# Kernel tuning notes

Measured on AMD Instinct MI355X. Metric: run time of the kernel, lower is better.

The kernel has to match this reference:

```python
import jax, jax.numpy as jnp
import numpy as np

N_EMBED = 1024
N_HEAD = 16
HEAD_DIM = N_EMBED // N_HEAD


def setup_inputs() -> dict:
    key = jax.random.key(0)
    ks = jax.random.split(key, 5)
    s = 1.0 / np.sqrt(N_EMBED)
    return {
        "x": jax.random.normal(ks[0], (4, 2048, N_EMBED), dtype=jnp.float32),
        "W_kqv": jax.random.normal(ks[1], (3 * N_EMBED, N_EMBED), dtype=jnp.float32) * s,
        "b_kqv": jax.random.normal(ks[2], (3 * N_EMBED,), dtype=jnp.float32) * s,
        "W_proj": jax.random.normal(ks[3], (N_EMBED, N_EMBED), dtype=jnp.float32) * s,
        "b_proj": jax.random.normal(ks[4], (N_EMBED,), dtype=jnp.float32) * s,
    }


def reference(x, W_kqv, b_kqv, W_proj, b_proj):
    B, S, E = x.shape
    H, D = N_HEAD, E // N_HEAD
    kqv = x @ W_kqv.T + b_kqv  # [B,S,3E]
    # torch code splits as k, q, v (in that order)
    k, q, v = jnp.split(kqv, 3, axis=-1)
    to_heads = lambda t: t.reshape(B, S, H, D).transpose(0, 2, 1, 3)  # [B,H,S,D]
    k, q, v = to_heads(k), to_heads(q), to_heads(v)
    scale = 1.0 / np.sqrt(D).astype(np.float32)
    attn = jnp.einsum("bhqd,bhkd->bhqk", q, k) * scale
    causal = jnp.tril(jnp.ones((S, S), dtype=bool))
    attn = jnp.where(causal, attn, -jnp.inf)
    attn = jax.nn.softmax(attn, axis=-1)
    # dropout: eval mode (identity) for deterministic reference
    y = jnp.einsum("bhqk,bhkd->bhqd", attn, v)
    y = y.transpose(0, 2, 1, 3).reshape(B, S, E)
    return y @ W_proj.T + b_proj
```

## Files before the change

kernel.cpp:

```cpp
#include <hip/hip_runtime.h>
#include <cstddef>
#include <cstdint>

#define EMB 1024
#define NH 16
#define HD 64
#define BATCH 4
#define SEQ 2048
#define MROWS (BATCH * SEQ)

typedef __attribute__((ext_vector_type(8))) short bf16x8;
typedef __attribute__((ext_vector_type(4))) float f32x4;

__device__ __forceinline__ unsigned short f2bf(float f) {
    union { float f; unsigned int i; } c; c.f = f;
    return (unsigned short)((c.i + 0x7FFFu + ((c.i >> 16) & 1u)) >> 16);
}
__device__ __forceinline__ unsigned short f2bfr(float f) {
    union { float f; unsigned int i; } c; c.f = f;
    return (unsigned short)((c.i + 0x8000u) >> 16);
}

#define GLOAD_LDS16(gp, lp) __builtin_amdgcn_global_load_lds(                  \
    (const __attribute__((address_space(1))) void*)(gp),                       \
    (__attribute__((address_space(3))) void*)(lp), 16, 0, 0)

__global__ __launch_bounds__(256) void cvt_all(
    const float* __restrict__ x, const float* __restrict__ wk,
    const float* __restrict__ wp, unsigned short* __restrict__ xh,
    unsigned short* __restrict__ wkh, unsigned short* __restrict__ wph) {
    const int A = (BATCH * SEQ * EMB) / 4;
    const int B2 = (3 * EMB * EMB) / 4;
    const int C = (EMB * EMB) / 4;
    const int tot = A + B2 + C;
    const int stride = gridDim.x * blockDim.x;
    for (int i = blockIdx.x * blockDim.x + threadIdx.x; i < tot; i += stride) {
        const float* s; unsigned short* d; int j;
        if (i < A)            { s = x;  d = xh;  j = i; }
        else if (i < A + B2)  { s = wk; d = wkh; j = i - A; }
        else                  { s = wp; d = wph; j = i - A - B2; }
        const float4 v = ((const float4*)s)[j];
        ushort4 h;
        h.x = f2bf(v.x); h.y = f2bf(v.y); h.z = f2bf(v.z); h.w = f2bf(v.w);
        ((ushort4*)d)[j] = h;
    }
}

__device__ __forceinline__ void stage_tile(const unsigned short* __restrict__ src,
                                           int row0, int kt,
                                           unsigned short* lds, int wave, int lane) {
#pragma unroll
    for (int i = 0; i < 2; ++i) {
        const int c = wave * 2 + i;
        const int r = c * 16 + (lane >> 2);
        const int kq = (lane & 3) * 8;
        GLOAD_LDS16(src + (size_t)(row0 + r) * 1024 + kt + kq, lds + c * 512);
    }
}

__global__ __launch_bounds__(256) void gemm_qkv_mfma(
    const unsigned short* __restrict__ xh, const unsigned short* __restrict__ wh,
    const float* __restrict__ bias,
    unsigned short* __restrict__ Ko, unsigned short* __restrict__ Qo,
    unsigned short* __restrict__ Vo) {
    __shared__ unsigned short Ah[128 * 32];
    __shared__ unsigned short Bh[128 * 32];

    const int t = threadIdx.x, lane = t & 63, w = t >> 6;
    const int wr = w >> 1, wc = w & 1;
    const int g8 = (lane >> 4) * 8, g4 = (lane >> 4) * 4, l15 = lane & 15;

    const int nwg = 64 * 24;
    const int lin = blockIdx.x + gridDim.x * blockIdx.y;
    const int swz = (lin & 7) * (nwg >> 3) + (lin >> 3);
    const int m0 = (swz & 63) * 128, n0 = (swz >> 6) * 128;

    f32x4 acc[4][4] = {};

    for (int kt = 0; kt < 1024; kt += 32) {
        stage_tile(xh, m0, kt, Ah, w, lane);
        stage_tile(wh, n0, kt, Bh, w, lane);
        __syncthreads();

        bf16x8 a[4], bb[4];
#pragma unroll
        for (int m = 0; m < 4; ++m)
            a[m] = *(const bf16x8*)&Ah[(wr * 64 + m * 16 + l15) * 32 + g8];
#pragma unroll
        for (int n = 0; n < 4; ++n)
            bb[n] = *(const bf16x8*)&Bh[(wc * 64 + n * 16 + l15) * 32 + g8];
#pragma unroll
        for (int m = 0; m < 4; ++m)
#pragma unroll
            for (int n = 0; n < 4; ++n)
                acc[m][n] = __builtin_amdgcn_mfma_f32_16x16x32_bf16(a[m], bb[n], acc[m][n], 0, 0, 0);
        __syncthreads();
    }

#pragma unroll
    for (int n = 0; n < 4; ++n) {
        const int col = n0 + wc * 64 + n * 16 + l15;
        const float bv = bias[col];
        const int which = col >> 10;
        unsigned short* outp = (which == 0) ? Ko : (which == 1 ? Qo : Vo);
        const int cm = col & 1023, h = cm >> 6, d = cm & 63;
#pragma unroll
        for (int m = 0; m < 4; ++m)
#pragma unroll
            for (int jj = 0; jj < 4; ++jj) {
                const int row = m0 + wr * 64 + m * 16 + g4 + jj;
                const int b = row >> 11, s = row & 2047;
                outp[(((size_t)(b * NH + h) * SEQ + s) << 6) + d] =
                    f2bf(acc[m][n][jj] + bv);
            }
    }
}

__global__ __launch_bounds__(256) void gemm_proj_mfma(
    const unsigned short* __restrict__ Yb, const unsigned short* __restrict__ wh,
    const float* __restrict__ bias, float* __restrict__ Out) {
    __shared__ unsigned short Ah[128 * 32];
    __shared__ unsigned short Bh[128 * 32];

    const int t = threadIdx.x, lane = t & 63, w = t >> 6;
    const int wr = w >> 1, wc = w & 1;
    const int g8 = (lane >> 4) * 8, g4 = (lane >> 4) * 4, l15 = lane & 15;

    const int nwg = 64 * 8;
    const int lin = blockIdx.x + gridDim.x * blockIdx.y;
    const int swz = (lin & 7) * (nwg >> 3) + (lin >> 3);
    const int m0 = (swz & 63) * 128, n0 = (swz >> 6) * 128;

    f32x4 acc[4][4] = {};

    for (int kt = 0; kt < 1024; kt += 32) {
        stage_tile(Yb, m0, kt, Ah, w, lane);
        stage_tile(wh, n0, kt, Bh, w, lane);
        __syncthreads();

        bf16x8 a[4], bb[4];
#pragma unroll
        for (int m = 0; m < 4; ++m)
            a[m] = *(const bf16x8*)&Ah[(wr * 64 + m * 16 + l15) * 32 + g8];
#pragma unroll
        for (int n = 0; n < 4; ++n)
            bb[n] = *(const bf16x8*)&Bh[(wc * 64 + n * 16 + l15) * 32 + g8];
#pragma unroll
        for (int m = 0; m < 4; ++m)
#pragma unroll
            for (int n = 0; n < 4; ++n)
                acc[m][n] = __builtin_amdgcn_mfma_f32_16x16x32_bf16(a[m], bb[n], acc[m][n], 0, 0, 0);
        __syncthreads();
    }

#pragma unroll
    for (int n = 0; n < 4; ++n) {
        const int col = n0 + wc * 64 + n * 16 + l15;
        const float bv = bias[col];
#pragma unroll
        for (int m = 0; m < 4; ++m)
#pragma unroll
            for (int jj = 0; jj < 4; ++jj) {
                const int row = m0 + wr * 64 + m * 16 + g4 + jj;
                Out[(size_t)row * EMB + col] = acc[m][n][jj] + bv;
            }
    }
}

__global__ __launch_bounds__(256, 2) void attn_mfma(
    const unsigned short* __restrict__ Kt, const unsigned short* __restrict__ Qt,
    const unsigned short* __restrict__ Vg, unsigned short* __restrict__ Y) {
    __shared__ unsigned short Ks[128][72];
    __shared__ unsigned short Vs[64][136];
    __shared__ unsigned short Ps[128][136];

    const int lin = blockIdx.x;
    const int swz = (lin & 7) * 64 + (lin >> 3);
    const int pair = swz & 7, bh = swz >> 3;
    const int b = bh >> 4, h = bh & 15;
    const unsigned short* Qp = Qt + ((size_t)bh * SEQ << 6);
    const unsigned short* Kp = Kt + ((size_t)bh * SEQ << 6);
    const unsigned short* Vp = Vg + ((size_t)bh * SEQ << 6);

    const int t = threadIdx.x, lane = t & 63, w = t >> 6;
    const int hi = lane >> 4, l15 = lane & 15, g8 = hi * 8;
    const float SCL = 0.125f * 1.44269504f;

    union U8 { uint4 q; unsigned short u[8]; };
    U8 kreg[4], vreg[4];
    auto loadKV = [&](int tile) {
#pragma unroll
        for (int i = 0; i < 4; ++i) {
            const int c = t + (i << 8);
            const int r = c >> 3, col = (c & 7) * 8;
            kreg[i].q = *(const uint4*)(Kp + ((size_t)tile << 13) + r * 64 + col);
            vreg[i].q = *(const uint4*)(Vp + ((size_t)tile << 13) + r * 64 + col);
        }
    };

#pragma unroll 1
    for (int ph = 0; ph < 2; ++ph) {
        const int qt = ph ? (15 - pair) : pair;
        const int ntiles = qt + 1;
        const int q0 = qt * 128 + w * 32;

        bf16x8 qf[2][2];
#pragma unroll
        for (int rb = 0; rb < 2; ++rb)
#pragma unroll
            for (int kc = 0; kc < 2; ++kc)
                qf[rb][kc] = *(const bf16x8*)(
                    Qp + ((size_t)(q0 + rb * 16 + l15) << 6) + kc * 32 + g8);

        float lsum[2] = {0.f, 0.f};
        f32x4 o_acc[2][4] = {};

        loadKV(0);
#pragma unroll 1
        for (int tile = 0; tile < ntiles; ++tile) {
            __syncthreads();
#pragma unroll
            for (int i = 0; i < 4; ++i) {
                const int c = t + (i << 8);
                const int r = c >> 3, col = (c & 7) * 8;
                *(uint4*)&Ks[r][col] = kreg[i].q;
#pragma unroll
                for (int j = 0; j < 8; ++j) {
                    const int d = col + j;
                    Vs[d][r ^ (d & 56)] = vreg[i].u[j];
                }
            }
            if (tile + 1 < ntiles) loadKV(tile + 1);
            __syncthreads();

            const bool diag = (tile == ntiles - 1);
            const int kvb = tile << 7;

            __builtin_amdgcn_s_setprio(1);
#pragma unroll
            for (int n = 0; n < 8; ++n) {
                const bf16x8 kf0 = *(const bf16x8*)&Ks[n * 16 + l15][g8];
                const bf16x8 kf1 = *(const bf16x8*)&Ks[n * 16 + l15][32 + g8];
                f32x4 t0 = {}, t1 = {};
                t0 = __builtin_amdgcn_mfma_f32_16x16x32_bf16(kf0, qf[0][0], t0, 0, 0, 0);
                t0 = __builtin_amdgcn_mfma_f32_16x16x32_bf16(kf1, qf[0][1], t0, 0, 0, 0);
                t1 = __builtin_amdgcn_mfma_f32_16x16x32_bf16(kf0, qf[1][0], t1, 0, 0, 0);
                t1 = __builtin_amdgcn_mfma_f32_16x16x32_bf16(kf1, qf[1][1], t1, 0, 0, 0);
#pragma unroll
                for (int rb = 0; rb < 2; ++rb) {
                    const f32x4 tt = rb ? t1 : t0;
                    const int qrow = q0 + rb * 16 + l15;
                    unsigned int pk[2];
#pragma unroll
                    for (int jp = 0; jp < 2; ++jp) {
                        float v0 = fmaf(tt[2 * jp], SCL, -8.0f);
                        float v1 = fmaf(tt[2 * jp + 1], SCL, -8.0f);
                        if (diag) {
                            const int kv = kvb + n * 16 + 4 * hi + 2 * jp;
                            if (kv > qrow)     v0 = -1e30f;
                            if (kv + 1 > qrow) v1 = -1e30f;
                        }
                        const float p0 = exp2f(v0), p1 = exp2f(v1);
                        lsum[rb] += p0 + p1;
                        pk[jp] = (unsigned int)f2bfr(p0) |
                                 ((unsigned int)f2bfr(p1) << 16);
                    }
                    *(uint2*)&Ps[w * 32 + rb * 16 + l15][n * 16 + 4 * hi] =
                        make_uint2(pk[0], pk[1]);
                }
            }

#pragma unroll
            for (int kc = 0; kc < 4; ++kc) {
                bf16x8 vf[4];
#pragma unroll
                for (int nd = 0; nd < 4; ++nd) {
                    const int d = nd * 16 + l15;
                    vf[nd] = *(const bf16x8*)&Vs[d][(kc * 32 + g8) ^ (d & 56)];
                }
                const bf16x8 pf0 = *(const bf16x8*)&Ps[w * 32 + l15][kc * 32 + g8];
                const bf16x8 pf1 = *(const bf16x8*)&Ps[w * 32 + 16 + l15][kc * 32 + g8];
#pragma unroll
                for (int nd = 0; nd < 4; ++nd) {
                    o_acc[0][nd] = __builtin_amdgcn_mfma_f32_16x16x32_bf16(pf0, vf[nd], o_acc[0][nd], 0, 0, 0);
                    o_acc[1][nd] = __builtin_amdgcn_mfma_f32_16x16x32_bf16(pf1, vf[nd], o_acc[1][nd], 0, 0, 0);
                }
            }
            __builtin_amdgcn_s_setprio(0);
        }

#pragma unroll
        for (int rb = 0; rb < 2; ++rb) {
            float lv = lsum[rb];
            lv += __shfl_xor(lv, 16);
            lv += __shfl_xor(lv, 32);
#pragma unroll
            for (int jj = 0; jj < 4; ++jj) {
                const float inv = 1.0f / __shfl(lv, 4 * hi + jj);
                const int srow = q0 + rb * 16 + 4 * hi + jj;
#pragma unroll
                for (int nd = 0; nd < 4; ++nd)
                    Y[((size_t)(b * SEQ + srow) << 10) + (h << 6) + nd * 16 + l15] =
                        f2bf(o_acc[rb][nd][jj] * inv);
            }
        }
    }
}

extern "C" void kernel_launch(void* const* d_in, const int* in_sizes, int n_in,
                              void* d_out, int out_size, void* d_ws, size_t ws_size,
                              hipStream_t stream) {
    const float* x  = (const float*)d_in[0];
    const float* Wk = (const float*)d_in[1];
    const float* bk = (const float*)d_in[2];
    const float* Wp = (const float*)d_in[3];
    const float* bp = (const float*)d_in[4];
    float* out = (float*)d_out;

    char* ws = (char*)d_ws;
    const size_t MB = 1024 * 1024;
    unsigned short* xh  = (unsigned short*)(ws + 0 * MB);
    unsigned short* wkh = (unsigned short*)(ws + 16 * MB);
    unsigned short* wph = (unsigned short*)(ws + 22 * MB);
    unsigned short* Ko  = (unsigned short*)(ws + 24 * MB);
    unsigned short* Qo  = (unsigned short*)(ws + 40 * MB);
    unsigned short* Vo  = (unsigned short*)(ws + 56 * MB);
    unsigned short* Yo  = (unsigned short*)(ws + 72 * MB);

    cvt_all<<<2048, 256, 0, stream>>>(x, Wk, Wp, xh, wkh, wph);

    gemm_qkv_mfma<<<dim3(MROWS / 128, 3072 / 128), 256, 0, stream>>>(
        xh, wkh, bk, Ko, Qo, Vo);
    attn_mfma<<<512, 256, 0, stream>>>(Ko, Qo, Vo, Yo);
    gemm_proj_mfma<<<dim3(MROWS / 128, EMB / 128), 256, 0, stream>>>(
        Yo, wph, bp, out);
}
```

Baseline: 282.9 us.

## Double-buffer GEMM LDS staging and halve attention P buffer for occupancy

Both GEMM kernels now double-buffer their LDS tiles, issuing the async global-to-LDS load of the next K-slice before computing on the current one. This drops one barrier per iteration and overlaps the loads with MFMA work. The attention kernel splits the 128-wide KV tile into two 64-column halves that reuse a P buffer half the previous size. That frees LDS so the launch bounds can rise to 3 workgroups per CU, at the cost of extra register pressure and a possible hazard if the P buffer is reused without a barrier between halves.

```diff
diff --git a/kernel.cpp b/kernel.cpp
--- a/kernel.cpp
+++ b/kernel.cpp
@@ -58,17 +58,55 @@
     }
 }
 
+__device__ __forceinline__ void gemm_2ph(const unsigned short* __restrict__ A,
+                                         const unsigned short* __restrict__ B,
+                                         unsigned short* As, unsigned short* Bs,
+                                         int m0, int n0, int w, int lane,
+                                         f32x4 (&acc)[4][4]) {
+    const int wr = w >> 1, wc = w & 1;
+    const int g8 = (lane >> 4) * 8, l15 = lane & 15;
+
+    stage_tile(A, m0, 0, As, w, lane);
+    stage_tile(B, n0, 0, Bs, w, lane);
+    __syncthreads();
+
+    int cur = 0;
+    for (int kt = 0; kt < 1024; kt += 32) {
+        const int nxt = cur ^ 1;
+        if (kt + 32 < 1024) {
+            stage_tile(A, m0, kt + 32, As + nxt * 4096, w, lane);
+            stage_tile(B, n0, kt + 32, Bs + nxt * 4096, w, lane);
+        }
+        const unsigned short* Ac = As + cur * 4096;
+        const unsigned short* Bc = Bs + cur * 4096;
+        bf16x8 a[4], bb[4];
+#pragma unroll
+        for (int m = 0; m < 4; ++m)
+            a[m] = *(const bf16x8*)&Ac[(wr * 64 + m * 16 + l15) * 32 + g8];
+#pragma unroll
+        for (int n = 0; n < 4; ++n)
+            bb[n] = *(const bf16x8*)&Bc[(wc * 64 + n * 16 + l15) * 32 + g8];
+#pragma unroll
+        for (int m = 0; m < 4; ++m)
+#pragma unroll
+            for (int n = 0; n < 4; ++n)
+                acc[m][n] = __builtin_amdgcn_mfma_f32_16x16x32_bf16(a[m], bb[n], acc[m][n], 0, 0, 0);
+        __syncthreads();
+        cur = nxt;
+    }
+}
+
 __global__ __launch_bounds__(256) void gemm_qkv_mfma(
     const unsigned short* __restrict__ xh, const unsigned short* __restrict__ wh,
     const float* __restrict__ bias,
     unsigned short* __restrict__ Ko, unsigned short* __restrict__ Qo,
     unsigned short* __restrict__ Vo) {
-    __shared__ unsigned short Ah[128 * 32];
-    __shared__ unsigned short Bh[128 * 32];
+    __shared__ unsigned short As[2 * 128 * 32];
+    __shared__ unsigned short Bs[2 * 128 * 32];
 
     const int t = threadIdx.x, lane = t & 63, w = t >> 6;
     const int wr = w >> 1, wc = w & 1;
-    const int g8 = (lane >> 4) * 8, g4 = (lane >> 4) * 4, l15 = lane & 15;
+    const int g4 = (lane >> 4) * 4, l15 = lane & 15;
 
     const int nwg = 64 * 24;
     const int lin = blockIdx.x + gridDim.x * blockIdx.y;
@@ -76,26 +114,7 @@
     const int m0 = (swz & 63) * 128, n0 = (swz >> 6) * 128;
 
     f32x4 acc[4][4] = {};
-
-    for (int kt = 0; kt < 1024; kt += 32) {
-        stage_tile(xh, m0, kt, Ah, w, lane);
-        stage_tile(wh, n0, kt, Bh, w, lane);
-        __syncthreads();
-
-        bf16x8 a[4], bb[4];
-#pragma unroll
-        for (int m = 0; m < 4; ++m)
-            a[m] = *(const bf16x8*)&Ah[(wr * 64 + m * 16 + l15) * 32 + g8];
-#pragma unroll
-        for (int n = 0; n < 4; ++n)
-            bb[n] = *(const bf16x8*)&Bh[(wc * 64 + n * 16 + l15) * 32 + g8];
-#pragma unroll
-        for (int m = 0; m < 4; ++m)
-#pragma unroll
-            for (int n = 0; n < 4; ++n)
-                acc[m][n] = __builtin_amdgcn_mfma_f32_16x16x32_bf16(a[m], bb[n], acc[m][n], 0, 0, 0);
-        __syncthreads();
-    }
+    gemm_2ph(xh, wh, As, Bs, m0, n0, w, lane, acc);
 
 #pragma unroll
     for (int n = 0; n < 4; ++n) {
@@ -119,12 +138,12 @@
 __global__ __launch_bounds__(256) void gemm_proj_mfma(
     const unsigned short* __restrict__ Yb, const unsigned short* __restrict__ wh,
     const float* __restrict__ bias, float* __restrict__ Out) {
-    __shared__ unsigned short Ah[128 * 32];
-    __shared__ unsigned short Bh[128 * 32];
+    __shared__ unsigned short As[2 * 128 * 32];
+    __shared__ unsigned short Bs[2 * 128 * 32];
 
     const int t = threadIdx.x, lane = t & 63, w = t >> 6;
     const int wr = w >> 1, wc = w & 1;
-    const int g8 = (lane >> 4) * 8, g4 = (lane >> 4) * 4, l15 = lane & 15;
+    const int g4 = (lane >> 4) * 4, l15 = lane & 15;
 
     const int nwg = 64 * 8;
     const int lin = blockIdx.x + gridDim.x * blockIdx.y;
@@ -132,26 +151,7 @@
     const int m0 = (swz & 63) * 128, n0 = (swz >> 6) * 128;
 
     f32x4 acc[4][4] = {};
-
-    for (int kt = 0; kt < 1024; kt += 32) {
-        stage_tile(Yb, m0, kt, Ah, w, lane);
-        stage_tile(wh, n0, kt, Bh, w, lane);
-        __syncthreads();
-
-        bf16x8 a[4], bb[4];
-#pragma unroll
-        for (int m = 0; m < 4; ++m)
-            a[m] = *(const bf16x8*)&Ah[(wr * 64 + m * 16 + l15) * 32 + g8];
-#pragma unroll
-        for (int n = 0; n < 4; ++n)
-            bb[n] = *(const bf16x8*)&Bh[(wc * 64 + n * 16 + l15) * 32 + g8];
-#pragma unroll
-        for (int m = 0; m < 4; ++m)
-#pragma unroll
-            for (int n = 0; n < 4; ++n)
-                acc[m][n] = __builtin_amdgcn_mfma_f32_16x16x32_bf16(a[m], bb[n], acc[m][n], 0, 0, 0);
-        __syncthreads();
-    }
+    gemm_2ph(Yb, wh, As, Bs, m0, n0, w, lane, acc);
 
 #pragma unroll
     for (int n = 0; n < 4; ++n) {
@@ -167,12 +167,12 @@
     }
 }
 
-__global__ __launch_bounds__(256, 2) void attn_mfma(
+__global__ __launch_bounds__(256, 3) void attn_mfma(
     const unsigned short* __restrict__ Kt, const unsigned short* __restrict__ Qt,
     const unsigned short* __restrict__ Vg, unsigned short* __restrict__ Y) {
     __shared__ unsigned short Ks[128][72];
     __shared__ unsigned short Vs[64][136];
-    __shared__ unsigned short Ps[128][136];
+    __shared__ unsigned short Ps[128][72];
 
     const int lin = blockIdx.x;
     const int swz = (lin & 7) * 64 + (lin >> 3);
@@ -238,52 +238,57 @@
 
             __builtin_amdgcn_s_setprio(1);
 #pragma unroll
-            for (int n = 0; n < 8; ++n) {
-                const bf16x8 kf0 = *(const bf16x8*)&Ks[n * 16 + l15][g8];
-                const bf16x8 kf1 = *(const bf16x8*)&Ks[n * 16 + l15][32 + g8];
-                f32x4 t0 = {}, t1 = {};
-                t0 = __builtin_amdgcn_mfma_f32_16x16x32_bf16(kf0, qf[0][0], t0, 0, 0, 0);
-                t0 = __builtin_amdgcn_mfma_f32_16x16x32_bf16(kf1, qf[0][1], t0, 0, 0, 0);
-                t1 = __builtin_amdgcn_mfma_f32_16x16x32_bf16(kf0, qf[1][0], t1, 0, 0, 0);
-                t1 = __builtin_amdgcn_mfma_f32_16x16x32_bf16(kf1, qf[1][1], t1, 0, 0, 0);
-#pragma unroll
-                for (int rb = 0; rb < 2; ++rb) {
-                    const f32x4 tt = rb ? t1 : t0;
-                    const int qrow = q0 + rb * 16 + l15;
-                    unsigned int pk[2];
-#pragma unroll
-                    for (int jp = 0; jp < 2; ++jp) {
-                        float v0 = fmaf(tt[2 * jp], SCL, -8.0f);
-                        float v1 = fmaf(tt[2 * jp + 1], SCL, -8.0f);
-                        if (diag) {
-                            const int kv = kvb + n * 16 + 4 * hi + 2 * jp;
-                            if (kv > qrow)     v0 = -1e30f;
-                            if (kv + 1 > qrow) v1 = -1e30f;
+            for (int half = 0; half < 2; ++half) {
+#pragma unroll
+                for (int nn = 0; nn < 4; ++nn) {
+                    const int n = half * 4 + nn;
+                    const bf16x8 kf0 = *(const bf16x8*)&Ks[n * 16 + l15][g8];
+                    const bf16x8 kf1 = *(const bf16x8*)&Ks[n * 16 + l15][32 + g8];
+                    f32x4 t0 = {}, t1 = {};
+                    t0 = __builtin_amdgcn_mfma_f32_16x16x32_bf16(kf0, qf[0][0], t0, 0, 0, 0);
+                    t0 = __builtin_amdgcn_mfma_f32_16x16x32_bf16(kf1, qf[0][1], t0, 0, 0, 0);
+                    t1 = __builtin_amdgcn_mfma_f32_16x16x32_bf16(kf0, qf[1][0], t1, 0, 0, 0);
+                    t1 = __builtin_amdgcn_mfma_f32_16x16x32_bf16(kf1, qf[1][1], t1, 0, 0, 0);
+#pragma unroll
+                    for (int rb = 0; rb < 2; ++rb) {
+                        const f32x4 tt = rb ? t1 : t0;
+                        const int qrow = q0 + rb * 16 + l15;
+                        unsigned int pk[2];
+#pragma unroll
+                        for (int jp = 0; jp < 2; ++jp) {
+                            float v0 = fmaf(tt[2 * jp], SCL, -8.0f);
+                            float v1 = fmaf(tt[2 * jp + 1], SCL, -8.0f);
+                            if (diag) {
+                                const int kv = kvb + n * 16 + 4 * hi + 2 * jp;
+                                if (kv > qrow)     v0 = -1e30f;
+                                if (kv + 1 > qrow) v1 = -1e30f;
+                            }
+                            const float p0 = exp2f(v0), p1 = exp2f(v1);
+                            lsum[rb] += p0 + p1;
+                            pk[jp] = (unsigned int)f2bfr(p0) |
+                                     ((unsigned int)f2bfr(p1) << 16);
                         }
-                        const float p0 = exp2f(v0), p1 = exp2f(v1);
-                        lsum[rb] += p0 + p1;
-                        pk[jp] = (unsigned int)f2bfr(p0) |
-                                 ((unsigned int)f2bfr(p1) << 16);
+                        *(uint2*)&Ps[w * 32 + rb * 16 + l15][nn * 16 + 4 * hi] =
+                            make_uint2(pk[0], pk[1]);
                     }
-                    *(uint2*)&Ps[w * 32 + rb * 16 + l15][n * 16 + 4 * hi] =
-                        make_uint2(pk[0], pk[1]);
                 }
-            }
-
-#pragma unroll
-            for (int kc = 0; kc < 4; ++kc) {
-                bf16x8 vf[4];
-#pragma unroll
-                for (int nd = 0; nd < 4; ++nd) {
-                    const int d = nd * 16 + l15;
-                    vf[nd] = *(const bf16x8*)&Vs[d][(kc * 32 + g8) ^ (d & 56)];
-                }
-                const bf16x8 pf0 = *(const bf16x8*)&Ps[w * 32 + l15][kc * 32 + g8];
-                const bf16x8 pf1 = *(const bf16x8*)&Ps[w * 32 + 16 + l15][kc * 32 + g8];
-#pragma unroll
-                for (int nd = 0; nd < 4; ++nd) {
-                    o_acc[0][nd] = __builtin_amdgcn_mfma_f32_16x16x32_bf16(pf0, vf[nd], o_acc[0][nd], 0, 0, 0);
-                    o_acc[1][nd] = __builtin_amdgcn_mfma_f32_16x16x32_bf16(pf1, vf[nd], o_acc[1][nd], 0, 0, 0);
+
+#pragma unroll
+                for (int kc2 = 0; kc2 < 2; ++kc2) {
+                    const int kc = half * 2 + kc2;
+                    bf16x8 vf[4];
+#pragma unroll
+                    for (int nd = 0; nd < 4; ++nd) {
+                        const int d = nd * 16 + l15;
+                        vf[nd] = *(const bf16x8*)&Vs[d][(kc * 32 + g8) ^ (d & 56)];
+                    }
+                    const bf16x8 pf0 = *(const bf16x8*)&Ps[w * 32 + l15][kc2 * 32 + g8];
+                    const bf16x8 pf1 = *(const bf16x8*)&Ps[w * 32 + 16 + l15][kc2 * 32 + g8];
+#pragma unroll
+                    for (int nd = 0; nd < 4; ++nd) {
+                        o_acc[0][nd] = __builtin_amdgcn_mfma_f32_16x16x32_bf16(pf0, vf[nd], o_acc[0][nd], 0, 0, 0);
+                        o_acc[1][nd] = __builtin_amdgcn_mfma_f32_16x16x32_bf16(pf1, vf[nd], o_acc[1][nd], 0, 0, 0);
+                    }
                 }
             }
             __builtin_amdgcn_s_setprio(0);
```

Result: slower. 318.1 us (+12.4%).
